# Optimization experiments

Hardware: AMD Instinct MI355X
Metric: run time of the kernel (lower is better)

Reference implementation:

```python
import jax, jax.numpy as jnp
import numpy as np

B, H, W, C = 2, 64, 64, 96
DIN, NST, RNK, K = 192, 16, 6, 4
L = H * W


def _make_ids():
    idx = np.arange(L).reshape(H, W)
    p0 = idx.reshape(-1)
    p1 = idx.T.reshape(-1)
    p2 = p0[::-1].copy()
    p3 = p1[::-1].copy()
    scan = np.stack([p0, p1, p2, p3]).astype(np.int32)
    inv = np.stack([np.argsort(p) for p in scan]).astype(np.int32)
    return jnp.asarray(scan), jnp.asarray(inv)


def setup_inputs() -> dict:
    key = jax.random.key(0)
    ks = jax.random.split(key, 10)
    scan_ids, inv_ids = _make_ids()
    std = RNK ** -0.5
    # dt bias init: inverse-softplus of dt ~ LogUniform(1e-3, 1e-1), as in VMM.dt_init
    u = jax.random.uniform(ks[5], (K, DIN))
    dt = jnp.exp(u * (np.log(0.1) - np.log(0.001)) + np.log(0.001))
    dt_b = dt + jnp.log(-jnp.expm1(-dt))
    return {
        "x": jax.random.normal(ks[0], (B, H, W, C), jnp.float32),
        "W_in": jax.random.normal(ks[1], (2 * DIN, C), jnp.float32) * 0.02,
        "conv_w": jax.random.normal(ks[2], (DIN, 1, 3, 3), jnp.float32) * 0.1,
        "conv_b": jnp.zeros((DIN,), jnp.float32),
        "x_proj_w": jax.random.normal(ks[3], (K, RNK + 2 * NST, DIN), jnp.float32) * 0.02,
        "dt_w": jax.random.uniform(ks[4], (K, DIN, RNK), jnp.float32, -std, std),
        "dt_b": dt_b.astype(jnp.float32),
        "A_logs": jnp.log(jnp.tile(jnp.arange(1, NST + 1, dtype=jnp.float32)[None], (K * DIN, 1))),
        "Ds": jnp.ones((K * DIN,), jnp.float32),
        "gate_w": jax.random.normal(ks[6], (4 * DIN, 4), jnp.float32) * 0.1,  # grouped 1x1 conv, groups=DIN
        "gate_b": jnp.zeros((4 * DIN,), jnp.float32),
        "ln_g": jnp.ones((DIN,), jnp.float32),
        "ln_b": jnp.zeros((DIN,), jnp.float32),
        "W_out": jax.random.normal(ks[7], (C, DIN), jnp.float32) * 0.02,
        "scan_ids": scan_ids,
        "inv_ids": inv_ids,
    }


def _forward(x, W_in, conv_w, conv_b, x_proj_w, dt_w, dt_b, A_logs, Ds, gate_w, gate_b, ln_g, ln_b, W_out, scan_ids, inv_ids):
    b, h, w, c = x.shape
    l = h * w
    din = conv_w.shape[0]
    k = x_proj_w.shape[0]
    nst = A_logs.shape[1]
    rnk = dt_w.shape[2]
    # in_proj + split into x / gate z
    xz = x @ W_in.T
    xc, z = jnp.split(xz, 2, axis=-1)
    xc = jnp.transpose(xc, (0, 3, 1, 2))  # (b, din, h, w)
    # depthwise 3x3 conv + SiLU
    xc = jax.lax.conv_general_dilated(
        xc, conv_w, (1, 1), "SAME", feature_group_count=din,
        dimension_numbers=("NCHW", "OIHW", "NCHW")) + conv_b[None, :, None, None]
    xc = jax.nn.silu(xc)
    # multi-directional gather (mair_ids_scan)
    xf = xc.reshape(b, din, l)
    xs = jnp.moveaxis(xf[:, :, scan_ids], 2, 1)  # (b, k, din, l)
    # x_proj (grouped 1x1 conv) -> dt, B, C
    x_dbl = jnp.einsum("bkdl,krd->bkrl", xs, x_proj_w)
    dts, Bs, Cs = jnp.split(x_dbl, [rnk, rnk + nst], axis=2)  # (b,k,rnk,l),(b,k,n,l),(b,k,n,l)
    delta = jax.nn.softplus(jnp.einsum("bkrl,kdr->bkdl", dts, dt_w) + dt_b[None, :, :, None])
    A = -jnp.exp(A_logs).reshape(k, din, nst)
    dA = jnp.exp(delta[..., None] * A[None, :, :, None, :])              # (b,k,d,l,n)
    dBu = (delta * xs)[..., None] * jnp.moveaxis(Bs, 2, 3)[:, :, None]   # (b,k,d,l,n)

    def step(hst, inp):
        da, dbu = inp
        hst = da * hst + dbu
        return hst, hst

    h0 = jnp.zeros((b, k, din, nst), jnp.float32)
    _, hs = jax.lax.scan(step, h0, (jnp.moveaxis(dA, 3, 0), jnp.moveaxis(dBu, 3, 0)))  # (l,b,k,d,n)
    ys = jnp.einsum("lbkdn,bknl->bkdl", hs, Cs) + xs * Ds.reshape(k, din)[None, :, :, None]
    # inverse scatter (mair_ids_inverse) + concat along channels
    y = jax.vmap(lambda yk, ik: yk[..., ik], in_axes=(1, 0), out_axes=1)(ys, inv_ids)
    y = y.reshape(b, k * din, h, w)
    # ShuffleAttn gating: group = din, group_channels = k
    shuf = y.reshape(b, k, din, h, w).transpose(0, 2, 1, 3, 4).reshape(b, k * din, h, w)
    pooled = shuf.mean(axis=(2, 3)).reshape(b, din, k)
    gate = jax.nn.sigmoid(jnp.einsum("bgi,goi->bgo", pooled, gate_w.reshape(din, k, k)) + gate_b.reshape(din, k))
    gate = gate.transpose(0, 2, 1).reshape(b, k * din)  # channel_rearrange
    y = y * gate[:, :, None, None]
    # sum the 4 direction branches
    y = y.reshape(b, k, din, h, w).sum(axis=1)
    y = jnp.transpose(y, (0, 2, 3, 1))  # (b,h,w,din)
    # LayerNorm(d_inner)
    mu = y.mean(-1, keepdims=True)
    var = ((y - mu) ** 2).mean(-1, keepdims=True)
    y = (y - mu) / jnp.sqrt(var + 1e-5) * ln_g + ln_b
    y = y * jax.nn.silu(z)
    return y @ W_out.T


def reference(x, W_in, conv_w, conv_b, x_proj_w, dt_w, dt_b, A_logs, Ds, gate_w, gate_b, ln_g, ln_b, W_out, scan_ids, inv_ids):
    return _forward(x, W_in, conv_w, conv_b, x_proj_w, dt_w, dt_b, A_logs, Ds, gate_w, gate_b, ln_g, ln_b, W_out, scan_ids, inv_ids)
```

## Files before the change

kernel.cpp:

```cpp
#include <hip/hip_runtime.h>
#include <math.h>

#define BB 2
#define CC 96
#define DIN 192
#define NST 16
#define RNK 6
#define KK 4
#define LL 4096
#define RTOT (RNK + 2*NST)


__global__ __launch_bounds__(256) void k_inproj(const float* __restrict__ x,
        const float* __restrict__ W_in, float* __restrict__ xc_pre,
        float* __restrict__ z_silu) {
    __shared__ float lx[96*33];
    __shared__ float wt[48*196];
    int b = blockIdx.y, z = blockIdx.z;
    int l0 = blockIdx.x * 32;
    int t = threadIdx.x;
    for (int i = 0; i < 3; ++i) {
        int e4 = t + 256*i;
        int c4 = e4 % 24, l = e4 / 24;
        float4 v = *(const float4*)&x[((size_t)(b*LL + l0 + l))*96 + 4*c4];
        lx[(4*c4+0)*33 + l] = v.x;
        lx[(4*c4+1)*33 + l] = v.y;
        lx[(4*c4+2)*33 + l] = v.z;
        lx[(4*c4+3)*33 + l] = v.w;
    }
    int lg = t & 7;
    int og = t >> 3;
    float acc[4][6];
    #pragma unroll
    for (int j = 0; j < 4; ++j)
        #pragma unroll
        for (int q = 0; q < 6; ++q) acc[j][q] = 0.f;
    for (int p = 0; p < 2; ++p) {
        __syncthreads();
        for (int i = 0; i < 9; ++i) {
            int e4 = t + 256*i;
            int cc4 = e4 % 12, oc = e4 / 12;
            float4 v = *(const float4*)&W_in[((size_t)(z*192 + oc))*96 + p*48 + 4*cc4];
            wt[(4*cc4+0)*196 + oc] = v.x;
            wt[(4*cc4+1)*196 + oc] = v.y;
            wt[(4*cc4+2)*196 + oc] = v.z;
            wt[(4*cc4+3)*196 + oc] = v.w;
        }
        __syncthreads();
        #pragma unroll 4
        for (int cc = 0; cc < 48; ++cc) {
            int c = p*48 + cc;
            float x0 = lx[c*33 + 4*lg + 0];
            float x1 = lx[c*33 + 4*lg + 1];
            float x2 = lx[c*33 + 4*lg + 2];
            float x3 = lx[c*33 + 4*lg + 3];
            const float* wr = &wt[cc*196 + 6*og];
            float2 w0 = *(const float2*)(wr);
            float2 w1 = *(const float2*)(wr + 2);
            float2 w2 = *(const float2*)(wr + 4);
            float wv[6] = {w0.x,w0.y, w1.x,w1.y, w2.x,w2.y};
            #pragma unroll
            for (int q = 0; q < 6; ++q) {
                acc[0][q] += x0*wv[q];
                acc[1][q] += x1*wv[q];
                acc[2][q] += x2*wv[q];
                acc[3][q] += x3*wv[q];
            }
        }
    }
    float* dst = (z == 0) ? xc_pre : z_silu;
    #pragma unroll
    for (int j = 0; j < 4; ++j) {
        int l = l0 + 4*lg + j;
        size_t base = (size_t)(b*LL + l)*DIN + 6*og;
        float v[6];
        #pragma unroll
        for (int q = 0; q < 6; ++q) {
            float a = acc[j][q];
            v[q] = z ? a/(1.f + __expf(-a)) : a;
        }
        *(float2*)&dst[base]     = make_float2(v[0], v[1]);
        *(float2*)&dst[base + 2] = make_float2(v[2], v[3]);
        *(float2*)&dst[base + 4] = make_float2(v[4], v[5]);
    }
}

__global__ __launch_bounds__(256) void k_conv(const float* __restrict__ xc,
        const float* __restrict__ cw, const float* __restrict__ cb,
        float* __restrict__ out) {
    int gid = blockIdx.x*256 + threadIdx.x;
    int dq = gid % 48;
    int r = gid / 48;
    int l = r & 4095, b = r >> 12;
    int w = l & 63, h = l >> 6;
    int d0 = dq*4;
    float4 acc = *(const float4*)&cb[d0];
    float wreg[4][9];
    #pragma unroll
    for (int j = 0; j < 4; ++j)
        #pragma unroll
        for (int tp = 0; tp < 9; ++tp) wreg[j][tp] = cw[(d0+j)*9 + tp];
    #pragma unroll
    for (int dh = -1; dh <= 1; ++dh) {
        int h2 = h + dh;
        bool okh = (h2 >= 0) && (h2 < 64);
        #pragma unroll
        for (int dw = -1; dw <= 1; ++dw) {
            int w2 = w + dw;
            if (okh && w2 >= 0 && w2 < 64) {
                float4 v = *(const float4*)&xc[((size_t)(b*LL + h2*64 + w2))*DIN + d0];
                int tp = (dh+1)*3 + (dw+1);
                acc.x += v.x*wreg[0][tp];
                acc.y += v.y*wreg[1][tp];
                acc.z += v.z*wreg[2][tp];
                acc.w += v.w*wreg[3][tp];
            }
        }
    }
    float4 o;
    o.x = acc.x/(1.f + __expf(-acc.x));
    o.y = acc.y/(1.f + __expf(-acc.y));
    o.z = acc.z/(1.f + __expf(-acc.z));
    o.w = acc.w/(1.f + __expf(-acc.w));
    *(float4*)&out[((size_t)(b*LL + l))*DIN + d0] = o;
}

__global__ __launch_bounds__(512) void k_proj(const float* __restrict__ xconv,
        const int* __restrict__ scan_ids, const float* __restrict__ xpw,
        float* __restrict__ dts, float* __restrict__ Bs, float* __restrict__ Cs) {
    __shared__ float lxs[96*65];
    __shared__ float lw[RTOT*96];
    __shared__ float lbc[64*33];
    __shared__ int lsid[64];
    int k = blockIdx.y, b = blockIdx.z;
    int l0 = blockIdx.x * 64;
    int t = threadIdx.x;
    if (t < 64) lsid[t] = scan_ids[k*LL + l0 + t];
    int l = t & 63;
    int rg = __builtin_amdgcn_readfirstlane(t >> 6);
    float acc[5];
    #pragma unroll
    for (int j = 0; j < 5; ++j) acc[j] = 0.f;
    for (int p = 0; p < 2; ++p) {
        __syncthreads();
        for (int i = 0; i < 3; ++i) {
            int e4 = t + 512*i;
            int dd4 = e4 % 24, ll = e4 / 24;
            float4 v = *(const float4*)&xconv[((size_t)(b*LL + lsid[ll]))*DIN + p*96 + 4*dd4];
            lxs[(4*dd4+0)*65 + ll] = v.x;
            lxs[(4*dd4+1)*65 + ll] = v.y;
            lxs[(4*dd4+2)*65 + ll] = v.z;
            lxs[(4*dd4+3)*65 + ll] = v.w;
        }
        for (int i = 0; i < 2; ++i) {
            int e4 = t + 512*i;
            if (e4 < RTOT*24) {
                int r = e4 / 24, dd4 = e4 % 24;
                *(float4*)&lw[r*96 + 4*dd4] =
                    *(const float4*)&xpw[(size_t)k*RTOT*DIN + r*DIN + p*96 + 4*dd4];
            }
        }
        __syncthreads();
        for (int dd = 0; dd < 96; dd += 4) {
            float x0 = lxs[(dd+0)*65 + l];
            float x1 = lxs[(dd+1)*65 + l];
            float x2 = lxs[(dd+2)*65 + l];
            float x3 = lxs[(dd+3)*65 + l];
            #pragma unroll
            for (int j = 0; j < 5; ++j) {
                int r = rg + 8*j;
                if (r < RTOT) {
                    float4 w = *(const float4*)&lw[r*96 + dd];
                    acc[j] += x0*w.x + x1*w.y + x2*w.z + x3*w.w;
                }
            }
        }
    }
    int bk = b*KK + k;
    #pragma unroll
    for (int j = 0; j < 5; ++j) {
        int r = rg + 8*j;
        if (r < RNK)       dts[((size_t)bk*LL + l0 + l)*8 + r] = acc[j];
        else if (r < RTOT) lbc[l*33 + (r - RNK)] = acc[j];
    }
    __syncthreads();
    size_t rowb = ((size_t)bk*LL + l0)*NST;
    for (int i = 0; i < 2; ++i) {
        int e = t + 512*i;
        int n = e & 15, ll = e >> 4;
        Bs[rowb + ll*NST + n] = lbc[ll*33 + n];
        Cs[rowb + ll*NST + n] = lbc[ll*33 + 16 + n];
    }
}

__global__ __launch_bounds__(384) void k_scan1(const float* __restrict__ xconv,
        const float* __restrict__ Bs, const float* __restrict__ Cs,
        const float* __restrict__ dts, const float* __restrict__ dtw,
        const float* __restrict__ dtb,
        const int* __restrict__ scan_ids, const float* __restrict__ A_logs,
        const float* __restrict__ Ds,
        float* __restrict__ y_dirs, float* __restrict__ segA,
        float* __restrict__ segB, int SL) {
    int seg = blockIdx.x, bk = blockIdx.y;
    int b = bk >> 2, k = bk & 3;
    int t = threadIdx.x;
    int half = t & 1, d = t >> 1;
    int l0 = seg * SL;
    float Av[8];
    {
        const float4* ap = (const float4*)(A_logs + ((k*DIN + d)*NST + half*8));
        float4 a0 = ap[0], a1 = ap[1];
        Av[0]=-__expf(a0.x); Av[1]=-__expf(a0.y); Av[2]=-__expf(a0.z); Av[3]=-__expf(a0.w);
        Av[4]=-__expf(a1.x); Av[5]=-__expf(a1.y); Av[6]=-__expf(a1.z); Av[7]=-__expf(a1.w);
    }
    float Av0 = -__expf(A_logs[(k*DIN + d)*NST]);
    bool okl = true;
    #pragma unroll
    for (int q = 0; q < 8; ++q) {
        float m = (float)(half*8 + q + 1);
        okl = okl && (fabsf(Av[q] - m*Av0) <= 1e-4f*m);
    }
    int fast = __all(okl);
    float Dv = Ds[k*DIN + d];
    float wdt[RNK];
    float bdt = dtb[k*DIN + d];
    #pragma unroll
    for (int r = 0; r < RNK; ++r) wdt[r] = dtw[(k*DIN + d)*RNK + r];
    float h[8];
    #pragma unroll
    for (int n = 0; n < 8; ++n) h[n] = 0.f;
    float sumdv = 0.f;
    const int* sid = scan_ids + k*LL + l0;
    const float* dbase = dts + ((size_t)bk*LL + l0)*8;
    const float* bbase = Bs + ((size_t)bk*LL + l0)*NST + half*8;
    const float* cbase = Cs + ((size_t)bk*LL + l0)*NST + half*8;
    int ln = sid[0];
    float xn = xconv[((size_t)(b*LL + ln))*DIN + d];
    float drc[RNK];
    #pragma unroll
    for (int r = 0; r < RNK; ++r) drc[r] = dbase[r];
    float4 bn0 = *(const float4*)bbase,      bn1 = *(const float4*)(bbase + 4);
    float4 cn0 = *(const float4*)cbase,      cn1 = *(const float4*)(cbase + 4);
    if (fast) {
        for (int li = 0; li < SL; ++li) {
            int l = ln;
            float xv = xn;
            float drv[RNK];
            #pragma unroll
            for (int r = 0; r < RNK; ++r) drv[r] = drc[r];
            float4 b0 = bn0, b1 = bn1, c0v = cn0, c1v = cn1;
            if (li + 1 < SL) {
                ln = sid[li + 1];
                xn = xconv[((size_t)(b*LL + ln))*DIN + d];
                #pragma unroll
                for (int r = 0; r < RNK; ++r) drc[r] = dbase[(li+1)*8 + r];
                bn0 = *(const float4*)(bbase + (size_t)(li+1)*NST);
                bn1 = *(const float4*)(bbase + (size_t)(li+1)*NST + 4);
                cn0 = *(const float4*)(cbase + (size_t)(li+1)*NST);
                cn1 = *(const float4*)(cbase + (size_t)(li+1)*NST + 4);
            }
            float aa = bdt;
            #pragma unroll
            for (int r = 0; r < RNK; ++r) aa += drv[r]*wdt[r];
            float dv = fmaxf(aa, 0.f) + __logf(1.f + __expf(-fabsf(aa)));
            sumdv += dv;
            float dxv = dv * xv;
            float bb[8] = {b0.x,b0.y,b0.z,b0.w, b1.x,b1.y,b1.z,b1.w};
            float cc[8] = {c0v.x,c0v.y,c0v.z,c0v.w, c1v.x,c1v.y,c1v.z,c1v.w};
            float E  = __expf(dv * Av0);
            float E2 = E*E, E4 = E2*E2;
            float P[8];
            P[0] = E;      P[1] = E2;     P[2] = E2*E;   P[3] = E4;
            P[4] = E4*E;   P[5] = E4*E2;  P[6] = E4*P[2]; P[7] = E4*E4;
            float s = half ? P[7] : 1.0f;
            float y = 0.f;
            #pragma unroll
            for (int n = 0; n < 8; ++n) {
                h[n] = (s*P[n])*h[n] + dxv*bb[n];
                y += h[n]*cc[n];
            }
            y += __shfl_xor(y, 1);
            if (half == 0) {
                y += xv * Dv;
                y_dirs[((size_t)(bk*LL + l))*DIN + d] = y;
            }
        }
    } else {
        for (int li = 0; li < SL; ++li) {
            int l = ln;
            float xv = xn;
            float drv[RNK];
            #pragma unroll
            for (int r = 0; r < RNK; ++r) drv[r] = drc[r];
            float4 b0 = bn0, b1 = bn1, c0v = cn0, c1v = cn1;
            if (li + 1 < SL) {
                ln = sid[li + 1];
                xn = xconv[((size_t)(b*LL + ln))*DIN + d];
                #pragma unroll
                for (int r = 0; r < RNK; ++r) drc[r] = dbase[(li+1)*8 + r];
                bn0 = *(const float4*)(bbase + (size_t)(li+1)*NST);
                bn1 = *(const float4*)(bbase + (size_t)(li+1)*NST + 4);
                cn0 = *(const float4*)(cbase + (size_t)(li+1)*NST);
                cn1 = *(const float4*)(cbase + (size_t)(li+1)*NST + 4);
            }
            float aa = bdt;
            #pragma unroll
            for (int r = 0; r < RNK; ++r) aa += drv[r]*wdt[r];
            float dv = fmaxf(aa, 0.f) + __logf(1.f + __expf(-fabsf(aa)));
            sumdv += dv;
            float dxv = dv * xv;
            float bb[8] = {b0.x,b0.y,b0.z,b0.w, b1.x,b1.y,b1.z,b1.w};
            float cc[8] = {c0v.x,c0v.y,c0v.z,c0v.w, c1v.x,c1v.y,c1v.z,c1v.w};
            float y = 0.f;
            #pragma unroll
            for (int n = 0; n < 8; ++n) {
                float e2 = __expf(dv * Av[n]);
                h[n] = e2*h[n] + dxv*bb[n];
                y += h[n]*cc[n];
            }
            y += __shfl_xor(y, 1);
            if (half == 0) {
                y += xv * Dv;
                y_dirs[((size_t)(bk*LL + l))*DIN + d] = y;
            }
        }
    }
    float a[8];
    #pragma unroll
    for (int n = 0; n < 8; ++n) a[n] = __expf(Av[n]*sumdv);
    size_t base = (((size_t)bk*gridDim.x + seg)*DIN + d)*NST + half*8;
    *(float4*)&segA[base]     = make_float4(a[0],a[1],a[2],a[3]);
    *(float4*)&segA[base + 4] = make_float4(a[4],a[5],a[6],a[7]);
    *(float4*)&segB[base]     = make_float4(h[0],h[1],h[2],h[3]);
    *(float4*)&segB[base + 4] = make_float4(h[4],h[5],h[6],h[7]);
}

__global__ __launch_bounds__(256) void k_scan2(const float* segA,
        const float* segB, float* hinit, float* poolsum, int SEGC) {
    int idx = blockIdx.x*256 + threadIdx.x;
    if (idx < BB*DIN*KK) poolsum[idx] = 0.f;
    if (idx >= BB*KK*DIN*NST) return;
    int bk = idx / (DIN*NST);
    int dn = idx % (DIN*NST);
    const size_t stride = DIN*NST;
    size_t o = (size_t)bk*SEGC*stride + dn;
    float h = 0.f;
    for (int s = 0; s < SEGC; s += 8) {
        float av[8], bv[8];
        #pragma unroll
        for (int j = 0; j < 8; ++j) {
            av[j] = segA[o + j*stride];
            bv[j] = segB[o + j*stride];
        }
        #pragma unroll
        for (int j = 0; j < 8; ++j) {
            hinit[o + j*stride] = h;
            h = av[j]*h + bv[j];
        }
        o += 8*stride;
    }
}

__global__ __launch_bounds__(384) void k_apply(const float* __restrict__ Cs,
        const float* __restrict__ dts, const float* __restrict__ dtw,
        const float* __restrict__ dtb,
        const int* __restrict__ scan_ids, const float* __restrict__ A_logs,
        const float* __restrict__ hinit,
        float* __restrict__ y_dirs, float* __restrict__ poolsum, int SL) {
    int seg = blockIdx.x, bk = blockIdx.y;
    int b = bk >> 2, k = bk & 3;
    int t = threadIdx.x;
    int half = t & 1, d = t >> 1;
    int l0 = seg * SL;
    float Av[8];
    {
        const float4* ap = (const float4*)(A_logs + ((k*DIN + d)*NST + half*8));
        float4 a0 = ap[0], a1 = ap[1];
        Av[0]=-__expf(a0.x); Av[1]=-__expf(a0.y); Av[2]=-__expf(a0.z); Av[3]=-__expf(a0.w);
        Av[4]=-__expf(a1.x); Av[5]=-__expf(a1.y); Av[6]=-__expf(a1.z); Av[7]=-__expf(a1.w);
    }
    float Av0 = -__expf(A_logs[(k*DIN + d)*NST]);
    bool okl = true;
    #pragma unroll
    for (int q = 0; q < 8; ++q) {
        float m = (float)(half*8 + q + 1);
        okl = okl && (fabsf(Av[q] - m*Av0) <= 1e-4f*m);
    }
    int fast = __all(okl);
    float h0[8];
    {
        size_t base = (((size_t)bk*gridDim.x + seg)*DIN + d)*NST + half*8;
        float4 v0 = *(const float4*)&hinit[base];
        float4 v1 = *(const float4*)&hinit[base + 4];
        h0[0]=v0.x; h0[1]=v0.y; h0[2]=v0.z; h0[3]=v0.w;
        h0[4]=v1.x; h0[5]=v1.y; h0[6]=v1.z; h0[7]=v1.w;
    }
    float wdt[RNK];
    float bdt = dtb[k*DIN + d];
    #pragma unroll
    for (int r = 0; r < RNK; ++r) wdt[r] = dtw[(k*DIN + d)*RNK + r];
    float cum = 0.f;
    float pool = 0.f;
    const int* sid = scan_ids + k*LL + l0;
    const float* dbase = dts + ((size_t)bk*LL + l0)*8;
    const float* cbase = Cs + ((size_t)bk*LL + l0)*NST + half*8;
    float drc[RNK];
    #pragma unroll
    for (int r = 0; r < RNK; ++r) drc[r] = dbase[r];
    float4 cn0 = *(const float4*)cbase, cn1 = *(const float4*)(cbase + 4);
    for (int li = 0; li < SL; ++li) {
        int l = sid[li];
        float drv[RNK];
        #pragma unroll
        for (int r = 0; r < RNK; ++r) drv[r] = drc[r];
        float4 c0v = cn0, c1v = cn1;
        if (li + 1 < SL) {
            #pragma unroll
            for (int r = 0; r < RNK; ++r) drc[r] = dbase[(li+1)*8 + r];
            cn0 = *(const float4*)(cbase + (size_t)(li+1)*NST);
            cn1 = *(const float4*)(cbase + (size_t)(li+1)*NST + 4);
        }
        float aa = bdt;
        #pragma unroll
        for (int r = 0; r < RNK; ++r) aa += drv[r]*wdt[r];
        cum += fmaxf(aa, 0.f) + __logf(1.f + __expf(-fabsf(aa)));
        float cc[8] = {c0v.x,c0v.y,c0v.z,c0v.w, c1v.x,c1v.y,c1v.z,c1v.w};
        float g;
        if (fast) {
            float E = __expf(Av0 * cum);
            g = 0.f;
            #pragma unroll
            for (int q = 7; q >= 0; --q) g = g*E + cc[q]*h0[q];
            g *= E;
            if (half) {
                float E2 = E*E, E4 = E2*E2;
                g *= E4*E4;
            }
        } else {
            g = 0.f;
            #pragma unroll
            for (int q = 0; q < 8; ++q)
                g += cc[q]*h0[q]*__expf(Av[q]*cum);
        }
        g += __shfl_xor(g, 1);
        if (half == 0) {
            size_t yo = ((size_t)(bk*LL + l))*DIN + d;
            float y = y_dirs[yo] + g;
            y_dirs[yo] = y;
            pool += y;
        }
    }
    if (half == 0) atomicAdd(&poolsum[(b*DIN + d)*KK + k], pool);
}

__global__ __launch_bounds__(256) void k_final(const float* __restrict__ y_dirs,
        const float* __restrict__ poolsum, const float* __restrict__ gw,
        const float* __restrict__ gb, const float* __restrict__ z_silu,
        const float* __restrict__ lng, const float* __restrict__ lnb,
        const float* __restrict__ Wout, float* __restrict__ out) {
    __shared__ float buf[16*196];
    __shared__ float lgate[DIN*KK];
    __shared__ float lwout[96*100];
    __shared__ float lmu[16], lrs[16];
    int b = blockIdx.y;
    int l0 = blockIdx.x * 16;
    int t = threadIdx.x;
    for (int e = t; e < DIN*KK; e += 256) {
        int d = e >> 2, o = e & 3;
        float acc = gb[d*KK + o];
        #pragma unroll
        for (int i = 0; i < KK; ++i)
            acc += (poolsum[(b*DIN + d)*KK + i] * (1.f/LL)) * gw[(d*KK + o)*KK + i];
        lgate[d*KK + o] = 1.f/(1.f + __expf(-acc));
    }
    __syncthreads();
    for (int i = 0; i < 3; ++i) {
        int e4 = t + 256*i;
        int d4 = e4 % 48, l = e4 / 48;
        int db = 4*d4;
        float4 acc = make_float4(0.f, 0.f, 0.f, 0.f);
        #pragma unroll
        for (int k = 0; k < KK; ++k) {
            float4 v = *(const float4*)&y_dirs[((size_t)((b*KK + k)*LL + l0 + l))*DIN + db];
            acc.x += v.x * lgate[(db+0)*KK + k];
            acc.y += v.y * lgate[(db+1)*KK + k];
            acc.z += v.z * lgate[(db+2)*KK + k];
            acc.w += v.w * lgate[(db+3)*KK + k];
        }
        *(float4*)&buf[l*196 + db] = acc;
    }
    __syncthreads();
    int l2 = t >> 4, q = t & 15;
    float s = 0.f, s2 = 0.f;
    for (int i = 0; i < 12; ++i) {
        float v = buf[l2*196 + q + 16*i];
        s += v; s2 += v*v;
    }
    s += __shfl_xor(s, 1);  s2 += __shfl_xor(s2, 1);
    s += __shfl_xor(s, 2);  s2 += __shfl_xor(s2, 2);
    s += __shfl_xor(s, 4);  s2 += __shfl_xor(s2, 4);
    s += __shfl_xor(s, 8);  s2 += __shfl_xor(s2, 8);
    if (q == 0) {
        float mu = s * (1.f/DIN);
        float var = s2 * (1.f/DIN) - mu*mu;
        lmu[l2] = mu;
        lrs[l2] = rsqrtf(var + 1e-5f);
    }
    __syncthreads();
    for (int i = 0; i < 3; ++i) {
        int e4 = t + 256*i;
        int d4 = e4 % 48, l = e4 / 48;
        int db = 4*d4;
        float4 v  = *(float4*)&buf[l*196 + db];
        float4 g4 = *(const float4*)&lng[db];
        float4 b4 = *(const float4*)&lnb[db];
        float4 z4 = *(const float4*)&z_silu[((size_t)(b*LL + l0 + l))*DIN + db];
        float mu = lmu[l], rs = lrs[l];
        v.x = ((v.x - mu)*rs*g4.x + b4.x) * z4.x;
        v.y = ((v.y - mu)*rs*g4.y + b4.y) * z4.y;
        v.z = ((v.z - mu)*rs*g4.z + b4.z) * z4.z;
        v.w = ((v.w - mu)*rs*g4.w + b4.w) * z4.w;
        *(float4*)&buf[l*196 + db] = v;
    }
    int l = t & 15;
    int c0 = (t >> 4) * 6;
    float acc[6];
    #pragma unroll
    for (int cc = 0; cc < 6; ++cc) acc[cc] = 0.f;
    for (int p = 0; p < 2; ++p) {
        __syncthreads();
        for (int i = 0; i < 9; ++i) {
            int e4 = t + 256*i;
            int dd4 = e4 % 24, cc = e4 / 24;
            *(float4*)&lwout[cc*100 + 4*dd4] =
                *(const float4*)&Wout[(size_t)cc*DIN + p*96 + 4*dd4];
        }
        __syncthreads();
        for (int d4 = 0; d4 < 24; ++d4) {
            float4 v = *(float4*)&buf[l*196 + p*96 + 4*d4];
            #pragma unroll
            for (int cc = 0; cc < 6; ++cc) {
                float4 w = *(const float4*)&lwout[(c0 + cc)*100 + 4*d4];
                acc[cc] += v.x*w.x + v.y*w.y + v.z*w.z + v.w*w.w;
            }
        }
    }
    #pragma unroll
    for (int cc = 0; cc < 6; ++cc)
        out[((size_t)(b*LL + l0 + l))*CC + c0 + cc] = acc[cc];
}

extern "C" void kernel_launch(void* const* d_in, const int* in_sizes, int n_in,
                              void* d_out, int out_size, void* d_ws, size_t ws_size,
                              hipStream_t stream) {
    const float* x      = (const float*)d_in[0];
    const float* W_in   = (const float*)d_in[1];
    const float* conv_w = (const float*)d_in[2];
    const float* conv_b = (const float*)d_in[3];
    const float* xpw    = (const float*)d_in[4];
    const float* dt_w   = (const float*)d_in[5];
    const float* dt_b   = (const float*)d_in[6];
    const float* A_logs = (const float*)d_in[7];
    const float* Ds     = (const float*)d_in[8];
    const float* gate_w = (const float*)d_in[9];
    const float* gate_b = (const float*)d_in[10];
    const float* ln_g   = (const float*)d_in[11];
    const float* ln_b   = (const float*)d_in[12];
    const float* W_out  = (const float*)d_in[13];
    const int* scan_ids = (const int*)d_in[14];
    float* out = (float*)d_out;

    const size_t baseF = 6291456ull + 2ull*1572864 + 262144ull + 2ull*524288 + 3072;
    int SEGC = 16;
    if ((baseF + 2ull*128*24576)*4 <= ws_size) SEGC = 128;
    else if ((baseF + 2ull*64*24576)*4 <= ws_size) SEGC = 64;
    else if ((baseF + 2ull*32*24576)*4 <= ws_size) SEGC = 32;
    int SL = LL / SEGC;
    size_t segF = (size_t)SEGC * 24576;

    float* ws      = (float*)d_ws;
    float* y_dirs  = ws;
    float* xc_pre  = ws;
    float* z_silu  = y_dirs  + 6291456;
    float* xconv   = z_silu  + 1572864;
    float* dts     = xconv   + 1572864;
    float* Bs      = dts     + 262144;
    float* Cs      = Bs      + 524288;
    float* poolsum = Cs      + 524288;
    float* segA    = poolsum + 3072;
    float* segB    = segA    + segF;
    float* hinit   = segA;

    k_inproj<<<dim3(LL/32, BB, 2), 256, 0, stream>>>(x, W_in, xc_pre, z_silu);
    k_conv<<<(BB*LL*48)/256, 256, 0, stream>>>(xc_pre, conv_w, conv_b, xconv);
    k_proj<<<dim3(LL/64, KK, BB), 512, 0, stream>>>(xconv, scan_ids, xpw,
                                                    dts, Bs, Cs);
    k_scan1<<<dim3(SEGC, BB*KK), 384, 0, stream>>>(xconv, Bs, Cs, dts, dt_w, dt_b,
                                                   scan_ids, A_logs, Ds,
                                                   y_dirs, segA, segB, SL);
    k_scan2<<<(BB*KK*DIN*NST + 255)/256, 256, 0, stream>>>(segA, segB, hinit,
                                                           poolsum, SEGC);
    k_apply<<<dim3(SEGC, BB*KK), 384, 0, stream>>>(Cs, dts, dt_w, dt_b,
                                                   scan_ids, A_logs, hinit,
                                                   y_dirs, poolsum, SL);
    k_final<<<dim3(LL/16, BB), 256, 0, stream>>>(y_dirs, poolsum, gate_w, gate_b,
                                                 z_silu, ln_g, ln_b, W_out, out);
}
```

Before: 276.5 us.

## Replace scan-id gathers with transposed conv copy and scan-order outputs

The conv kernel now also writes a transposed (w-major) copy of its output. The projection and scan kernels then read rows at affine positions (forward, reversed, or from the transposed copy) instead of looking up scan_ids, so the index-load dependency disappears from the sequential loop. Scan outputs are stored in scan order, and the final kernel computes the inverse permutation arithmetically when it gathers the four directions. In exchange there is an extra 6 MB buffer write and a larger workspace, and the code hard-codes the four scan orders rather than reading the scan_ids input.

```diff
diff --git a/kernel.cpp b/kernel.cpp
--- a/kernel.cpp
+++ b/kernel.cpp
@@ -87,7 +87,7 @@
 
 __global__ __launch_bounds__(256) void k_conv(const float* __restrict__ xc,
         const float* __restrict__ cw, const float* __restrict__ cb,
-        float* __restrict__ out) {
+        float* __restrict__ out, float* __restrict__ outT) {
     int gid = blockIdx.x*256 + threadIdx.x;
     int dq = gid % 48;
     int r = gid / 48;
@@ -123,19 +123,22 @@
     o.z = acc.z/(1.f + __expf(-acc.z));
     o.w = acc.w/(1.f + __expf(-acc.w));
     *(float4*)&out[((size_t)(b*LL + l))*DIN + d0] = o;
+    int lt = w*64 + h;
+    *(float4*)&outT[((size_t)(b*LL + lt))*DIN + d0] = o;
 }
 
 __global__ __launch_bounds__(512) void k_proj(const float* __restrict__ xconv,
-        const int* __restrict__ scan_ids, const float* __restrict__ xpw,
+        const float* __restrict__ xconvT, const float* __restrict__ xpw,
         float* __restrict__ dts, float* __restrict__ Bs, float* __restrict__ Cs) {
     __shared__ float lxs[96*65];
     __shared__ float lw[RTOT*96];
     __shared__ float lbc[64*33];
-    __shared__ int lsid[64];
     int k = blockIdx.y, b = blockIdx.z;
     int l0 = blockIdx.x * 64;
     int t = threadIdx.x;
-    if (t < 64) lsid[t] = scan_ids[k*LL + l0 + t];
+    const float* src = (k & 1) ? xconvT : xconv;
+    int rb = (k < 2) ? l0 : (LL - 1 - l0);
+    int rs = (k < 2) ? 1 : -1;
     int l = t & 63;
     int rg = __builtin_amdgcn_readfirstlane(t >> 6);
     float acc[5];
@@ -146,7 +149,8 @@
         for (int i = 0; i < 3; ++i) {
             int e4 = t + 512*i;
             int dd4 = e4 % 24, ll = e4 / 24;
-            float4 v = *(const float4*)&xconv[((size_t)(b*LL + lsid[ll]))*DIN + p*96 + 4*dd4];
+            int row = rb + rs*ll;
+            float4 v = *(const float4*)&src[((size_t)(b*LL + row))*DIN + p*96 + 4*dd4];
             lxs[(4*dd4+0)*65 + ll] = v.x;
             lxs[(4*dd4+1)*65 + ll] = v.y;
             lxs[(4*dd4+2)*65 + ll] = v.z;
@@ -194,18 +198,21 @@
 }
 
 __global__ __launch_bounds__(384) void k_scan1(const float* __restrict__ xconv,
+        const float* __restrict__ xconvT,
         const float* __restrict__ Bs, const float* __restrict__ Cs,
         const float* __restrict__ dts, const float* __restrict__ dtw,
         const float* __restrict__ dtb,
-        const int* __restrict__ scan_ids, const float* __restrict__ A_logs,
-        const float* __restrict__ Ds,
-        float* __restrict__ y_dirs, float* __restrict__ segA,
+        const float* __restrict__ A_logs, const float* __restrict__ Ds,
+        float* __restrict__ y_scan, float* __restrict__ segA,
         float* __restrict__ segB, int SL) {
     int seg = blockIdx.x, bk = blockIdx.y;
     int b = bk >> 2, k = bk & 3;
     int t = threadIdx.x;
     int half = t & 1, d = t >> 1;
     int l0 = seg * SL;
+    const float* src = (k & 1) ? xconvT : xconv;
+    int rb = (k < 2) ? l0 : (LL - 1 - l0);
+    int rs = (k < 2) ? 1 : -1;
     float Av[8];
     {
         const float4* ap = (const float4*)(A_logs + ((k*DIN + d)*NST + half*8));
@@ -230,12 +237,10 @@
     #pragma unroll
     for (int n = 0; n < 8; ++n) h[n] = 0.f;
     float sumdv = 0.f;
-    const int* sid = scan_ids + k*LL + l0;
     const float* dbase = dts + ((size_t)bk*LL + l0)*8;
     const float* bbase = Bs + ((size_t)bk*LL + l0)*NST + half*8;
     const float* cbase = Cs + ((size_t)bk*LL + l0)*NST + half*8;
-    int ln = sid[0];
-    float xn = xconv[((size_t)(b*LL + ln))*DIN + d];
+    float xn = src[((size_t)(b*LL + rb))*DIN + d];
     float drc[RNK];
     #pragma unroll
     for (int r = 0; r < RNK; ++r) drc[r] = dbase[r];
@@ -243,15 +248,14 @@
     float4 cn0 = *(const float4*)cbase,      cn1 = *(const float4*)(cbase + 4);
     if (fast) {
         for (int li = 0; li < SL; ++li) {
-            int l = ln;
             float xv = xn;
             float drv[RNK];
             #pragma unroll
             for (int r = 0; r < RNK; ++r) drv[r] = drc[r];
             float4 b0 = bn0, b1 = bn1, c0v = cn0, c1v = cn1;
             if (li + 1 < SL) {
-                ln = sid[li + 1];
-                xn = xconv[((size_t)(b*LL + ln))*DIN + d];
+                int row = rb + rs*(li + 1);
+                xn = src[((size_t)(b*LL + row))*DIN + d];
                 #pragma unroll
                 for (int r = 0; r < RNK; ++r) drc[r] = dbase[(li+1)*8 + r];
                 bn0 = *(const float4*)(bbase + (size_t)(li+1)*NST);
@@ -270,7 +274,7 @@
             float E  = __expf(dv * Av0);
             float E2 = E*E, E4 = E2*E2;
             float P[8];
-            P[0] = E;      P[1] = E2;     P[2] = E2*E;   P[3] = E4;
+            P[0] = E;      P[1] = E2;     P[2] = E2*E;    P[3] = E4;
             P[4] = E4*E;   P[5] = E4*E2;  P[6] = E4*P[2]; P[7] = E4*E4;
             float s = half ? P[7] : 1.0f;
             float y = 0.f;
@@ -282,20 +286,19 @@
             y += __shfl_xor(y, 1);
             if (half == 0) {
                 y += xv * Dv;
-                y_dirs[((size_t)(bk*LL + l))*DIN + d] = y;
+                y_scan[((size_t)(bk*LL + l0 + li))*DIN + d] = y;
             }
         }
     } else {
         for (int li = 0; li < SL; ++li) {
-            int l = ln;
             float xv = xn;
             float drv[RNK];
             #pragma unroll
             for (int r = 0; r < RNK; ++r) drv[r] = drc[r];
             float4 b0 = bn0, b1 = bn1, c0v = cn0, c1v = cn1;
             if (li + 1 < SL) {
-                ln = sid[li + 1];
-                xn = xconv[((size_t)(b*LL + ln))*DIN + d];
+                int row = rb + rs*(li + 1);
+                xn = src[((size_t)(b*LL + row))*DIN + d];
                 #pragma unroll
                 for (int r = 0; r < RNK; ++r) drc[r] = dbase[(li+1)*8 + r];
                 bn0 = *(const float4*)(bbase + (size_t)(li+1)*NST);
@@ -321,7 +324,7 @@
             y += __shfl_xor(y, 1);
             if (half == 0) {
                 y += xv * Dv;
-                y_dirs[((size_t)(bk*LL + l))*DIN + d] = y;
+                y_scan[((size_t)(bk*LL + l0 + li))*DIN + d] = y;
             }
         }
     }
@@ -364,9 +367,8 @@
 __global__ __launch_bounds__(384) void k_apply(const float* __restrict__ Cs,
         const float* __restrict__ dts, const float* __restrict__ dtw,
         const float* __restrict__ dtb,
-        const int* __restrict__ scan_ids, const float* __restrict__ A_logs,
-        const float* __restrict__ hinit,
-        float* __restrict__ y_dirs, float* __restrict__ poolsum, int SL) {
+        const float* __restrict__ A_logs, const float* __restrict__ hinit,
+        float* __restrict__ y_scan, float* __restrict__ poolsum, int SL) {
     int seg = blockIdx.x, bk = blockIdx.y;
     int b = bk >> 2, k = bk & 3;
     int t = threadIdx.x;
@@ -401,7 +403,6 @@
     for (int r = 0; r < RNK; ++r) wdt[r] = dtw[(k*DIN + d)*RNK + r];
     float cum = 0.f;
     float pool = 0.f;
-    const int* sid = scan_ids + k*LL + l0;
     const float* dbase = dts + ((size_t)bk*LL + l0)*8;
     const float* cbase = Cs + ((size_t)bk*LL + l0)*NST + half*8;
     float drc[RNK];
@@ -409,7 +410,6 @@
     for (int r = 0; r < RNK; ++r) drc[r] = dbase[r];
     float4 cn0 = *(const float4*)cbase, cn1 = *(const float4*)(cbase + 4);
     for (int li = 0; li < SL; ++li) {
-        int l = sid[li];
         float drv[RNK];
         #pragma unroll
         for (int r = 0; r < RNK; ++r) drv[r] = drc[r];
@@ -444,16 +444,16 @@
         }
         g += __shfl_xor(g, 1);
         if (half == 0) {
-            size_t yo = ((size_t)(bk*LL + l))*DIN + d;
-            float y = y_dirs[yo] + g;
-            y_dirs[yo] = y;
+            size_t yo = ((size_t)(bk*LL + l0 + li))*DIN + d;
+            float y = y_scan[yo] + g;
+            y_scan[yo] = y;
             pool += y;
         }
     }
     if (half == 0) atomicAdd(&poolsum[(b*DIN + d)*KK + k], pool);
 }
 
-__global__ __launch_bounds__(256) void k_final(const float* __restrict__ y_dirs,
+__global__ __launch_bounds__(256) void k_final(const float* __restrict__ y_scan,
         const float* __restrict__ poolsum, const float* __restrict__ gw,
         const float* __restrict__ gb, const float* __restrict__ z_silu,
         const float* __restrict__ lng, const float* __restrict__ lnb,
@@ -478,10 +478,13 @@
         int e4 = t + 256*i;
         int d4 = e4 % 48, l = e4 / 48;
         int db = 4*d4;
+        int ls = l0 + l;
+        int tpl = ((ls & 63) << 6) | (ls >> 6);
+        int pk[4] = {ls, tpl, LL - 1 - ls, LL - 1 - tpl};
         float4 acc = make_float4(0.f, 0.f, 0.f, 0.f);
         #pragma unroll
         for (int k = 0; k < KK; ++k) {
-            float4 v = *(const float4*)&y_dirs[((size_t)((b*KK + k)*LL + l0 + l))*DIN + db];
+            float4 v = *(const float4*)&y_scan[((size_t)((b*KK + k)*LL + pk[k]))*DIN + db];
             acc.x += v.x * lgate[(db+0)*KK + k];
             acc.y += v.y * lgate[(db+1)*KK + k];
             acc.z += v.z * lgate[(db+2)*KK + k];
@@ -567,10 +570,9 @@
     const float* ln_g   = (const float*)d_in[11];
     const float* ln_b   = (const float*)d_in[12];
     const float* W_out  = (const float*)d_in[13];
-    const int* scan_ids = (const int*)d_in[14];
     float* out = (float*)d_out;
 
-    const size_t baseF = 6291456ull + 2ull*1572864 + 262144ull + 2ull*524288 + 3072;
+    const size_t baseF = 6291456ull + 3ull*1572864 + 262144ull + 2ull*524288 + 3072;
     int SEGC = 16;
     if ((baseF + 2ull*128*24576)*4 <= ws_size) SEGC = 128;
     else if ((baseF + 2ull*64*24576)*4 <= ws_size) SEGC = 64;
@@ -579,11 +581,12 @@
     size_t segF = (size_t)SEGC * 24576;
 
     float* ws      = (float*)d_ws;
-    float* y_dirs  = ws;
+    float* y_scan  = ws;
     float* xc_pre  = ws;
-    float* z_silu  = y_dirs  + 6291456;
+    float* z_silu  = y_scan  + 6291456;
     float* xconv   = z_silu  + 1572864;
-    float* dts     = xconv   + 1572864;
+    float* xconvT  = xconv   + 1572864;
+    float* dts     = xconvT  + 1572864;
     float* Bs      = dts     + 262144;
     float* Cs      = Bs      + 524288;
     float* poolsum = Cs      + 524288;
@@ -592,17 +595,18 @@
     float* hinit   = segA;
 
     k_inproj<<<dim3(LL/32, BB, 2), 256, 0, stream>>>(x, W_in, xc_pre, z_silu);
-    k_conv<<<(BB*LL*48)/256, 256, 0, stream>>>(xc_pre, conv_w, conv_b, xconv);
-    k_proj<<<dim3(LL/64, KK, BB), 512, 0, stream>>>(xconv, scan_ids, xpw,
+    k_conv<<<(BB*LL*48)/256, 256, 0, stream>>>(xc_pre, conv_w, conv_b,
+                                               xconv, xconvT);
+    k_proj<<<dim3(LL/64, KK, BB), 512, 0, stream>>>(xconv, xconvT, xpw,
                                                     dts, Bs, Cs);
-    k_scan1<<<dim3(SEGC, BB*KK), 384, 0, stream>>>(xconv, Bs, Cs, dts, dt_w, dt_b,
-                                                   scan_ids, A_logs, Ds,
-                                                   y_dirs, segA, segB, SL);
+    k_scan1<<<dim3(SEGC, BB*KK), 384, 0, stream>>>(xconv, xconvT, Bs, Cs, dts,
+                                                   dt_w, dt_b, A_logs, Ds,
+                                                   y_scan, segA, segB, SL);
     k_scan2<<<(BB*KK*DIN*NST + 255)/256, 256, 0, stream>>>(segA, segB, hinit,
                                                            poolsum, SEGC);
     k_apply<<<dim3(SEGC, BB*KK), 384, 0, stream>>>(Cs, dts, dt_w, dt_b,
-                                                   scan_ids, A_logs, hinit,
-                                                   y_dirs, poolsum, SL);
-    k_final<<<dim3(LL/16, BB), 256, 0, stream>>>(y_dirs, poolsum, gate_w, gate_b,
+                                                   A_logs, hinit,
+                                                   y_scan, poolsum, SL);
+    k_final<<<dim3(LL/16, BB), 256, 0, stream>>>(y_scan, poolsum, gate_w, gate_b,
                                                  z_silu, ln_g, ln_b, W_out, out);
 }
```

Result: slower. 282.6 us (+2.2%).
